# Performance work log

Hardware: AMD Instinct MI355X
Metric: run time of the kernel (lower is better)

The kernel has to match this reference:

```python
import jax, jax.numpy as jnp
import numpy as np

E, C, H, I = 8, 4096, 1024, 4096

def setup_inputs() -> dict:
    key = jax.random.key(0)
    k_x, k_g, k_u, k_d = jax.random.split(key, 4)
    scale_h = 1.0 / np.sqrt(H)
    scale_i = 1.0 / np.sqrt(I)
    return {
        "x_routed": jax.random.normal(k_x, (E, C, H), dtype=jnp.float32),
        "W_gate": jax.random.normal(k_g, (E, H, I), dtype=jnp.float32) * scale_h,
        "W_up": jax.random.normal(k_u, (E, H, I), dtype=jnp.float32) * scale_h,
        "W_down": jax.random.normal(k_d, (E, I, H), dtype=jnp.float32) * scale_i,
    }

def reference(x_routed, W_gate, W_up, W_down):
    # Per-expert SwiGLU MLP, batched over the expert axis as a grouped GEMM.
    # gate = silu(x @ Wg); up = x @ Wu; out = (gate * up) @ Wd
    gate = jax.nn.silu(jnp.einsum("ech,ehi->eci", x_routed, W_gate))
    up = jnp.einsum("ech,ehi->eci", x_routed, W_up)
    out = jnp.einsum("eci,eih->ech", gate * up, W_down)
    return out
```

## Files before the change

kernel.cpp:

```cpp
#include <hip/hip_runtime.h>
#include <hip/hip_bf16.h>
#include <stdint.h>
#include <stddef.h>

#define E_ 8
#define C_ 4096
#define H_ 1024
#define I_ 4096

typedef short s16;
typedef __attribute__((ext_vector_type(8))) short short8;
typedef __attribute__((ext_vector_type(4))) float f32x4;
typedef __attribute__((ext_vector_type(4))) float float4v;

__device__ __forceinline__ s16 f2bf(float f) {
  union { __hip_bfloat16 h; s16 s; } u;
  u.h = __float2bfloat16(f);
  return u.s;
}

__device__ __forceinline__ void gload16(const void* gsrc, void* ldst) {
  __builtin_amdgcn_global_load_lds(
      (const __attribute__((address_space(1))) void*)gsrc,
      (__attribute__((address_space(3))) void*)ldst, 16, 0, 0);
}

__global__ __launch_bounds__(256) void prep_kernel(
    const float* __restrict__ x, const float* __restrict__ Wg,
    const float* __restrict__ Wu, const float* __restrict__ Wd,
    s16* __restrict__ xb, s16* __restrict__ Wgu, s16* __restrict__ WdT)
{
  __shared__ float tile[64][65];
  const int t = threadIdx.x;
  const int z = blockIdx.z;
  const size_t e = blockIdx.y;

  if (z == 0) {
    size_t base = e * (size_t)C_ * H_ + ((size_t)blockIdx.x * 256 + t) * 16;
    for (int j = 0; j < 16; j += 8) {
      float4v v0 = *(const float4v*)(x + base + j);
      float4v v1 = *(const float4v*)(x + base + j + 4);
      s16 o[8];
      o[0] = f2bf(v0[0]); o[1] = f2bf(v0[1]); o[2] = f2bf(v0[2]); o[3] = f2bf(v0[3]);
      o[4] = f2bf(v1[0]); o[5] = f2bf(v1[1]); o[6] = f2bf(v1[2]); o[7] = f2bf(v1[3]);
      *(short8*)(xb + base + j) = *(short8*)o;
    }
    return;
  }

  const float* src; int Cc;
  if (z == 1)      { src = Wg + e * (size_t)H_ * I_; Cc = I_; }
  else if (z == 2) { src = Wu + e * (size_t)H_ * I_; Cc = I_; }
  else             { src = Wd + e * (size_t)H_ * I_; Cc = H_; }

  const int tpr  = Cc >> 6;
  const int trow = blockIdx.x / tpr;
  const int tcol = blockIdx.x % tpr;

  const int c = t & 63, rq = t >> 6;
  for (int i = 0; i < 16; ++i) {
    int r = rq * 16 + i;
    tile[r][c] = src[(size_t)(trow * 64 + r) * Cc + tcol * 64 + c];
  }
  __syncthreads();

  const int ro = t >> 2, cb = (t & 3) * 16;
  s16 o[16];
  for (int j = 0; j < 16; ++j) o[j] = f2bf(tile[cb + j][ro]);

  const int i0 = tcol * 64 + ro;
  s16* op;
  if (z == 3) {
    op = WdT + e * (size_t)H_ * I_ + (size_t)i0 * I_ + trow * 64 + cb;
  } else {
    int grow = ((i0 & ~15) << 1) + (i0 & 15) + ((z == 2) ? 16 : 0);
    op = Wgu + e * (size_t)2 * I_ * H_ + (size_t)grow * H_ + trow * 64 + cb;
  }
  *(short8*)op       = *(short8*)&o[0];
  *(short8*)(op + 8) = *(short8*)&o[8];
}

#define LDAF(B, MH, M, CX) \
  (*(const short8*)(shm + (B)*16384 + ((wm + (MH)*64 + (M)*16 + lr) << 6) + (CX)))
#define LDBF(B, N, CX) \
  (*(const short8*)(shm + 32768 + (B)*16384 + ((wn + (N)*16 + lr) << 6) + (CX)))

#define MFMA16(MH, A0, A1, A2, A3)                                                            \
  acc[(MH)*4+0][0] = __builtin_amdgcn_mfma_f32_16x16x32_bf16(A0, bf[0], acc[(MH)*4+0][0],0,0,0); \
  acc[(MH)*4+0][1] = __builtin_amdgcn_mfma_f32_16x16x32_bf16(A0, bf[1], acc[(MH)*4+0][1],0,0,0); \
  acc[(MH)*4+0][2] = __builtin_amdgcn_mfma_f32_16x16x32_bf16(A0, bf[2], acc[(MH)*4+0][2],0,0,0); \
  acc[(MH)*4+0][3] = __builtin_amdgcn_mfma_f32_16x16x32_bf16(A0, bf[3], acc[(MH)*4+0][3],0,0,0); \
  acc[(MH)*4+1][0] = __builtin_amdgcn_mfma_f32_16x16x32_bf16(A1, bf[0], acc[(MH)*4+1][0],0,0,0); \
  acc[(MH)*4+1][1] = __builtin_amdgcn_mfma_f32_16x16x32_bf16(A1, bf[1], acc[(MH)*4+1][1],0,0,0); \
  acc[(MH)*4+1][2] = __builtin_amdgcn_mfma_f32_16x16x32_bf16(A1, bf[2], acc[(MH)*4+1][2],0,0,0); \
  acc[(MH)*4+1][3] = __builtin_amdgcn_mfma_f32_16x16x32_bf16(A1, bf[3], acc[(MH)*4+1][3],0,0,0); \
  acc[(MH)*4+2][0] = __builtin_amdgcn_mfma_f32_16x16x32_bf16(A2, bf[0], acc[(MH)*4+2][0],0,0,0); \
  acc[(MH)*4+2][1] = __builtin_amdgcn_mfma_f32_16x16x32_bf16(A2, bf[1], acc[(MH)*4+2][1],0,0,0); \
  acc[(MH)*4+2][2] = __builtin_amdgcn_mfma_f32_16x16x32_bf16(A2, bf[2], acc[(MH)*4+2][2],0,0,0); \
  acc[(MH)*4+2][3] = __builtin_amdgcn_mfma_f32_16x16x32_bf16(A2, bf[3], acc[(MH)*4+2][3],0,0,0); \
  acc[(MH)*4+3][0] = __builtin_amdgcn_mfma_f32_16x16x32_bf16(A3, bf[0], acc[(MH)*4+3][0],0,0,0); \
  acc[(MH)*4+3][1] = __builtin_amdgcn_mfma_f32_16x16x32_bf16(A3, bf[1], acc[(MH)*4+3][1],0,0,0); \
  acc[(MH)*4+3][2] = __builtin_amdgcn_mfma_f32_16x16x32_bf16(A3, bf[2], acc[(MH)*4+3][2],0,0,0); \
  acc[(MH)*4+3][3] = __builtin_amdgcn_mfma_f32_16x16x32_bf16(A3, bf[3], acc[(MH)*4+3][3],0,0,0);

#define VMW4 asm volatile("s_waitcnt vmcnt(4)" ::: "memory");

#define PHASE(B, MH, CX, RDB, STMT, WV)                                      \
  {                                                                          \
    short8 af0 = LDAF(B, MH, 0, CX);                                         \
    short8 af1 = LDAF(B, MH, 1, CX);                                         \
    short8 af2 = LDAF(B, MH, 2, CX);                                         \
    short8 af3 = LDAF(B, MH, 3, CX);                                         \
    if (RDB) {                                                               \
      bf[0] = LDBF(B, 0, CX); bf[1] = LDBF(B, 1, CX);                        \
      bf[2] = LDBF(B, 2, CX); bf[3] = LDBF(B, 3, CX);                        \
    }                                                                        \
    STMT                                                                     \
    __builtin_amdgcn_sched_barrier(0);                                       \
    __builtin_amdgcn_s_barrier();                                            \
    asm volatile("s_waitcnt lgkmcnt(0)" ::: "memory");                       \
    __builtin_amdgcn_sched_barrier(0);                                       \
    __builtin_amdgcn_s_setprio(1);                                           \
    MFMA16(MH, af0, af1, af2, af3)                                           \
    __builtin_amdgcn_s_setprio(0);                                           \
    __builtin_amdgcn_sched_barrier(0);                                       \
    WV                                                                       \
    __builtin_amdgcn_s_barrier();                                            \
  }

template<bool GATEUP>
__global__ __launch_bounds__(512, 2) void gemm256(
    const s16* __restrict__ Abase, const s16* __restrict__ Bbase,
    s16* __restrict__ HOut, float* __restrict__ FOut)
{
  constexpr int K  = GATEUP ? H_ : I_;
  constexpr int NB = GATEUP ? 2 * I_ : H_;
  constexpr int NT = K / 64;
  constexpr int TN = NB / 256;
  constexpr int TM = C_ / 256;
  constexpr int NWG = TM * TN;

  __shared__ s16 shm[65536];

  const int tid  = threadIdx.x;
  const int wave = tid >> 6, lane = tid & 63;
  const int e    = blockIdx.z;

  const int bid = blockIdx.x;
  int bm, bn;
  if constexpr (GATEUP) {
    const int xcd = bid & 7;
    const int idx = bid >> 3;
    bn = (xcd & 3) * 8 + (idx & 7);
    bm = (xcd >> 2) * 8 + (idx >> 3);
  } else {
    const int swz = (bid & 7) * (NWG / 8) + (bid >> 3);
    bm = swz / TN; bn = swz % TN;
  }

  const s16* A = Abase + (size_t)e * C_ * K + (size_t)bm * 256 * K;
  const s16* B = Bbase + (size_t)e * NB * K + (size_t)bn * 256 * K;

  const int wm  = (wave >> 2) * 128;
  const int wn  = (wave & 3) * 64;
  const int lr  = lane & 15;
  const int lkb = (lane >> 4) * 8;
  const int xr  = (lr & 7) << 3;
  const int cx0 = lkb ^ xr;
  const int cx1 = (32 + lkb) ^ xr;

  const int srow = tid >> 3;
  const int scol = ((tid & 7) ^ (srow & 7)) * 8;
  const size_t stoff = (size_t)srow * K + scol;
  const int sdst = wave * 512;

  auto stageA = [&](int kt, int b) {
    #pragma unroll
    for (int h = 0; h < 2; ++h)
      #pragma unroll
      for (int l = 0; l < 2; ++l)
        gload16(A + (size_t)(h * 128 + l * 64) * K + (size_t)kt * 64 + stoff,
                shm + b * 16384 + h * 8192 + l * 4096 + sdst);
  };
  auto stageB = [&](int kt, int b) {
    #pragma unroll
    for (int h = 0; h < 2; ++h)
      #pragma unroll
      for (int l = 0; l < 2; ++l)
        gload16(B + (size_t)(h * 128 + l * 64) * K + (size_t)kt * 64 + stoff,
                shm + 32768 + b * 16384 + h * 8192 + l * 4096 + sdst);
  };

  f32x4 acc[8][4];
  #pragma unroll
  for (int m = 0; m < 8; ++m)
    #pragma unroll
    for (int n = 0; n < 4; ++n) acc[m][n] = (f32x4){0.f, 0.f, 0.f, 0.f};

  stageB(0, 0);
  stageA(0, 0);
  stageB(1, 1);
  asm volatile("s_waitcnt vmcnt(4)" ::: "memory");
  __builtin_amdgcn_sched_barrier(0);
  __builtin_amdgcn_s_barrier();

  short8 bf[4];
  for (int i = 0; i < NT / 2; ++i) {
    const int t1 = 2 * i + 1;
    const int t2 = (2 * i + 2 < NT) ? (2 * i + 2) : (NT - 1);
    const int t3 = (2 * i + 3 < NT) ? (2 * i + 3) : (NT - 1);
    PHASE(0, 0, cx0, 1, { stageA(t1, 1); }, )
    PHASE(0, 1, cx0, 0, {}, )
    PHASE(0, 0, cx1, 1, {}, )
    PHASE(0, 1, cx1, 0, { stageB(t2, 0); }, VMW4)
    PHASE(1, 0, cx0, 1, { stageA(t2, 0); }, )
    PHASE(1, 1, cx0, 0, {}, )
    PHASE(1, 0, cx1, 1, {}, )
    PHASE(1, 1, cx1, 0, { stageB(t3, 1); }, VMW4)
  }

  const int lq = (lane >> 4) * 4;
  if constexpr (GATEUP) {
    s16* Hp = HOut + (size_t)e * C_ * I_;
    const int ibase = bn * 128 + (wn >> 1);
    #pragma unroll
    for (int m = 0; m < 8; ++m) {
      const int row = bm * 256 + wm + m * 16 + lq;
      #pragma unroll
      for (int p = 0; p < 2; ++p) {
        const int col = ibase + p * 16 + lr;
        s16* hp = Hp + (size_t)row * I_ + col;
        #pragma unroll
        for (int j = 0; j < 4; ++j) {
          float g = acc[m][2 * p][j], u = acc[m][2 * p + 1][j];
          float sg = 1.0f / (1.0f + __expf(-g));
          hp[(size_t)j * I_] = f2bf(g * sg * u);
        }
      }
    }
  } else {
    float* Op = FOut + (size_t)e * C_ * H_;
    #pragma unroll
    for (int m = 0; m < 8; ++m) {
      const int row = bm * 256 + wm + m * 16 + lq;
      #pragma unroll
      for (int n = 0; n < 4; ++n) {
        const int col = bn * 256 + wn + n * 16 + lr;
        #pragma unroll
        for (int j = 0; j < 4; ++j)
          Op[(size_t)(row + j) * H_ + col] = acc[m][n][j];
      }
    }
  }
}

extern "C" void kernel_launch(void* const* d_in, const int* in_sizes, int n_in,
                              void* d_out, int out_size, void* d_ws, size_t ws_size,
                              hipStream_t stream) {
  const float* x  = (const float*)d_in[0];
  const float* Wg = (const float*)d_in[1];
  const float* Wu = (const float*)d_in[2];
  const float* Wd = (const float*)d_in[3];
  float* out = (float*)d_out;

  const size_t szX  = (size_t)C_ * H_;
  const size_t szGU = (size_t)2 * I_ * H_;
  const size_t szWd = (size_t)H_ * I_;
  const size_t szH  = (size_t)C_ * I_;

  const size_t needFull = 2 * E_ * (szX + szGU + szWd + szH);

  if (ws_size >= needFull) {
    s16* xb  = (s16*)d_ws;
    s16* Wgu = xb  + E_ * szX;
    s16* WdT = Wgu + E_ * szGU;
    s16* hbf = WdT + E_ * szWd;

    prep_kernel<<<dim3(1024, E_, 4), 256, 0, stream>>>(
        x, Wg, Wu, Wd, xb, Wgu, WdT);
    gemm256<true><<<dim3((C_/256)*(2*I_/256), 1, E_), 512, 0, stream>>>(
        xb, Wgu, hbf, nullptr);
    gemm256<false><<<dim3((C_/256)*(H_/256), 1, E_), 512, 0, stream>>>(
        hbf, WdT, nullptr, out);
  } else {
    s16* xb  = (s16*)d_ws;
    s16* Wgu = xb  + szX;
    s16* WdT = Wgu + szGU;
    s16* hbf = WdT + szWd;

    for (int e = 0; e < E_; ++e) {
      prep_kernel<<<dim3(1024, 1, 4), 256, 0, stream>>>(
          x + e * szX, Wg + e * szWd, Wu + e * szWd, Wd + e * szWd,
          xb, Wgu, WdT);
      gemm256<true><<<dim3((C_/256)*(2*I_/256), 1, 1), 512, 0, stream>>>(
          xb, Wgu, hbf, nullptr);
      gemm256<false><<<dim3((C_/256)*(H_/256), 1, 1), 512, 0, stream>>>(
          hbf, WdT, nullptr, out + e * szX);
    }
  }
}
```

Before: 965.4 us.

## Software-pipeline LDS fragment reads one phase ahead with partial lgkmcnt waits

After: 970.2 us. About the same (+0.5%).

```diff
diff --git a/kernel.cpp b/kernel.cpp
--- a/kernel.cpp
+++ b/kernel.cpp
@@ -85,43 +85,43 @@
 #define LDBF(B, N, CX) \
   (*(const short8*)(shm + 32768 + (B)*16384 + ((wn + (N)*16 + lr) << 6) + (CX)))
 
-#define MFMA16(MH, A0, A1, A2, A3)                                                            \
-  acc[(MH)*4+0][0] = __builtin_amdgcn_mfma_f32_16x16x32_bf16(A0, bf[0], acc[(MH)*4+0][0],0,0,0); \
-  acc[(MH)*4+0][1] = __builtin_amdgcn_mfma_f32_16x16x32_bf16(A0, bf[1], acc[(MH)*4+0][1],0,0,0); \
-  acc[(MH)*4+0][2] = __builtin_amdgcn_mfma_f32_16x16x32_bf16(A0, bf[2], acc[(MH)*4+0][2],0,0,0); \
-  acc[(MH)*4+0][3] = __builtin_amdgcn_mfma_f32_16x16x32_bf16(A0, bf[3], acc[(MH)*4+0][3],0,0,0); \
-  acc[(MH)*4+1][0] = __builtin_amdgcn_mfma_f32_16x16x32_bf16(A1, bf[0], acc[(MH)*4+1][0],0,0,0); \
-  acc[(MH)*4+1][1] = __builtin_amdgcn_mfma_f32_16x16x32_bf16(A1, bf[1], acc[(MH)*4+1][1],0,0,0); \
-  acc[(MH)*4+1][2] = __builtin_amdgcn_mfma_f32_16x16x32_bf16(A1, bf[2], acc[(MH)*4+1][2],0,0,0); \
-  acc[(MH)*4+1][3] = __builtin_amdgcn_mfma_f32_16x16x32_bf16(A1, bf[3], acc[(MH)*4+1][3],0,0,0); \
-  acc[(MH)*4+2][0] = __builtin_amdgcn_mfma_f32_16x16x32_bf16(A2, bf[0], acc[(MH)*4+2][0],0,0,0); \
-  acc[(MH)*4+2][1] = __builtin_amdgcn_mfma_f32_16x16x32_bf16(A2, bf[1], acc[(MH)*4+2][1],0,0,0); \
-  acc[(MH)*4+2][2] = __builtin_amdgcn_mfma_f32_16x16x32_bf16(A2, bf[2], acc[(MH)*4+2][2],0,0,0); \
-  acc[(MH)*4+2][3] = __builtin_amdgcn_mfma_f32_16x16x32_bf16(A2, bf[3], acc[(MH)*4+2][3],0,0,0); \
-  acc[(MH)*4+3][0] = __builtin_amdgcn_mfma_f32_16x16x32_bf16(A3, bf[0], acc[(MH)*4+3][0],0,0,0); \
-  acc[(MH)*4+3][1] = __builtin_amdgcn_mfma_f32_16x16x32_bf16(A3, bf[1], acc[(MH)*4+3][1],0,0,0); \
-  acc[(MH)*4+3][2] = __builtin_amdgcn_mfma_f32_16x16x32_bf16(A3, bf[2], acc[(MH)*4+3][2],0,0,0); \
-  acc[(MH)*4+3][3] = __builtin_amdgcn_mfma_f32_16x16x32_bf16(A3, bf[3], acc[(MH)*4+3][3],0,0,0);
+#define RD_A(DST, B, MH, CX)                                                 \
+  DST[0] = LDAF(B, MH, 0, CX); DST[1] = LDAF(B, MH, 1, CX);                  \
+  DST[2] = LDAF(B, MH, 2, CX); DST[3] = LDAF(B, MH, 3, CX);
+
+#define RD_B(DST, B, CX)                                                     \
+  DST[0] = LDBF(B, 0, CX); DST[1] = LDBF(B, 1, CX);                          \
+  DST[2] = LDBF(B, 2, CX); DST[3] = LDBF(B, 3, CX);
+
+#define MFMA16S(MH, AF, BF)                                                                     \
+  acc[(MH)*4+0][0] = __builtin_amdgcn_mfma_f32_16x16x32_bf16(AF[0], BF[0], acc[(MH)*4+0][0],0,0,0); \
+  acc[(MH)*4+0][1] = __builtin_amdgcn_mfma_f32_16x16x32_bf16(AF[0], BF[1], acc[(MH)*4+0][1],0,0,0); \
+  acc[(MH)*4+0][2] = __builtin_amdgcn_mfma_f32_16x16x32_bf16(AF[0], BF[2], acc[(MH)*4+0][2],0,0,0); \
+  acc[(MH)*4+0][3] = __builtin_amdgcn_mfma_f32_16x16x32_bf16(AF[0], BF[3], acc[(MH)*4+0][3],0,0,0); \
+  acc[(MH)*4+1][0] = __builtin_amdgcn_mfma_f32_16x16x32_bf16(AF[1], BF[0], acc[(MH)*4+1][0],0,0,0); \
+  acc[(MH)*4+1][1] = __builtin_amdgcn_mfma_f32_16x16x32_bf16(AF[1], BF[1], acc[(MH)*4+1][1],0,0,0); \
+  acc[(MH)*4+1][2] = __builtin_amdgcn_mfma_f32_16x16x32_bf16(AF[1], BF[2], acc[(MH)*4+1][2],0,0,0); \
+  acc[(MH)*4+1][3] = __builtin_amdgcn_mfma_f32_16x16x32_bf16(AF[1], BF[3], acc[(MH)*4+1][3],0,0,0); \
+  acc[(MH)*4+2][0] = __builtin_amdgcn_mfma_f32_16x16x32_bf16(AF[2], BF[0], acc[(MH)*4+2][0],0,0,0); \
+  acc[(MH)*4+2][1] = __builtin_amdgcn_mfma_f32_16x16x32_bf16(AF[2], BF[1], acc[(MH)*4+2][1],0,0,0); \
+  acc[(MH)*4+2][2] = __builtin_amdgcn_mfma_f32_16x16x32_bf16(AF[2], BF[2], acc[(MH)*4+2][2],0,0,0); \
+  acc[(MH)*4+2][3] = __builtin_amdgcn_mfma_f32_16x16x32_bf16(AF[2], BF[3], acc[(MH)*4+2][3],0,0,0); \
+  acc[(MH)*4+3][0] = __builtin_amdgcn_mfma_f32_16x16x32_bf16(AF[3], BF[0], acc[(MH)*4+3][0],0,0,0); \
+  acc[(MH)*4+3][1] = __builtin_amdgcn_mfma_f32_16x16x32_bf16(AF[3], BF[1], acc[(MH)*4+3][1],0,0,0); \
+  acc[(MH)*4+3][2] = __builtin_amdgcn_mfma_f32_16x16x32_bf16(AF[3], BF[2], acc[(MH)*4+3][2],0,0,0); \
+  acc[(MH)*4+3][3] = __builtin_amdgcn_mfma_f32_16x16x32_bf16(AF[3], BF[3], acc[(MH)*4+3][3],0,0,0);
 
 #define VMW4 asm volatile("s_waitcnt vmcnt(4)" ::: "memory");
 
-#define PHASE(B, MH, CX, RDB, STMT, WV)                                      \
+#define PH(TOP, LGKM, MH, AF, BF, WV)                                        \
   {                                                                          \
-    short8 af0 = LDAF(B, MH, 0, CX);                                         \
-    short8 af1 = LDAF(B, MH, 1, CX);                                         \
-    short8 af2 = LDAF(B, MH, 2, CX);                                         \
-    short8 af3 = LDAF(B, MH, 3, CX);                                         \
-    if (RDB) {                                                               \
-      bf[0] = LDBF(B, 0, CX); bf[1] = LDBF(B, 1, CX);                        \
-      bf[2] = LDBF(B, 2, CX); bf[3] = LDBF(B, 3, CX);                        \
-    }                                                                        \
-    STMT                                                                     \
+    TOP                                                                      \
     __builtin_amdgcn_sched_barrier(0);                                       \
     __builtin_amdgcn_s_barrier();                                            \
-    asm volatile("s_waitcnt lgkmcnt(0)" ::: "memory");                       \
+    asm volatile("s_waitcnt lgkmcnt(" #LGKM ")" ::: "memory");               \
     __builtin_amdgcn_sched_barrier(0);                                       \
     __builtin_amdgcn_s_setprio(1);                                           \
-    MFMA16(MH, af0, af1, af2, af3)                                           \
+    MFMA16S(MH, AF, BF)                                                      \
     __builtin_amdgcn_s_setprio(0);                                           \
     __builtin_amdgcn_sched_barrier(0);                                       \
     WV                                                                       \
@@ -204,19 +204,27 @@
   __builtin_amdgcn_sched_barrier(0);
   __builtin_amdgcn_s_barrier();
 
-  short8 bf[4];
+  short8 afA[4], afB[4], bfA[4], bfB[4];
   for (int i = 0; i < NT / 2; ++i) {
     const int t1 = 2 * i + 1;
     const int t2 = (2 * i + 2 < NT) ? (2 * i + 2) : (NT - 1);
     const int t3 = (2 * i + 3 < NT) ? (2 * i + 3) : (NT - 1);
-    PHASE(0, 0, cx0, 1, { stageA(t1, 1); }, )
-    PHASE(0, 1, cx0, 0, {}, )
-    PHASE(0, 0, cx1, 1, {}, )
-    PHASE(0, 1, cx1, 0, { stageB(t2, 0); }, VMW4)
-    PHASE(1, 0, cx0, 1, { stageA(t2, 0); }, )
-    PHASE(1, 1, cx0, 0, {}, )
-    PHASE(1, 0, cx1, 1, {}, )
-    PHASE(1, 1, cx1, 0, { stageB(t3, 1); }, VMW4)
+    PH({ RD_A(afA,0,0,cx0) RD_B(bfA,0,cx0) RD_A(afB,0,1,cx0) stageA(t1,1); },
+       4, 0, afA, bfA, )
+    PH({ RD_A(afA,0,0,cx1) RD_B(bfB,0,cx1) },
+       8, 1, afB, bfA, )
+    PH({ RD_A(afB,0,1,cx1) },
+       4, 0, afA, bfB, )
+    PH({ stageB(t2,0); },
+       0, 1, afB, bfB, VMW4)
+    PH({ RD_A(afA,1,0,cx0) RD_B(bfA,1,cx0) RD_A(afB,1,1,cx0) stageA(t2,0); },
+       4, 0, afA, bfA, )
+    PH({ RD_A(afA,1,0,cx1) RD_B(bfB,1,cx1) },
+       8, 1, afB, bfA, )
+    PH({ RD_A(afB,1,1,cx1) },
+       4, 0, afA, bfB, )
+    PH({ stageB(t3,1); },
+       0, 1, afB, bfB, VMW4)
   }
 
   const int lq = (lane >> 4) * 4;
```

## Process several N tiles per workgroup with continuous K-pipeline across tiles

Applied to the files above, without the earlier changes.

Measured after the change: 981.0 us. About the same (+1.6%).

```diff
diff --git a/kernel.cpp b/kernel.cpp
--- a/kernel.cpp
+++ b/kernel.cpp
@@ -128,17 +128,19 @@
     __builtin_amdgcn_s_barrier();                                            \
   }
 
-template<bool GATEUP>
+template<bool GATEUP, int NTILES>
 __global__ __launch_bounds__(512, 2) void gemm256(
     const s16* __restrict__ Abase, const s16* __restrict__ Bbase,
     s16* __restrict__ HOut, float* __restrict__ FOut)
 {
-  constexpr int K  = GATEUP ? H_ : I_;
-  constexpr int NB = GATEUP ? 2 * I_ : H_;
-  constexpr int NT = K / 64;
-  constexpr int TN = NB / 256;
-  constexpr int TM = C_ / 256;
-  constexpr int NWG = TM * TN;
+  constexpr int K     = GATEUP ? H_ : I_;
+  constexpr int NB    = GATEUP ? 2 * I_ : H_;
+  constexpr int NT    = K / 64;
+  constexpr int LOGNT = GATEUP ? 4 : 6;
+  constexpr int TN    = NB / 256;
+  constexpr int TNC   = TN / NTILES;
+  constexpr int TM    = C_ / 256;
+  constexpr int VMAX  = NTILES * NT - 1;
 
   __shared__ s16 shm[65536];
 
@@ -147,19 +149,19 @@
   const int e    = blockIdx.z;
 
   const int bid = blockIdx.x;
-  int bm, bn;
+  int bm, bnc;
   if constexpr (GATEUP) {
     const int xcd = bid & 7;
     const int idx = bid >> 3;
-    bn = (xcd & 3) * 8 + (idx & 7);
-    bm = (xcd >> 2) * 8 + (idx >> 3);
+    bnc = (xcd & 3) * 2 + (idx & 1);
+    bm  = (xcd >> 2) * 8 + (idx >> 1);
   } else {
-    const int swz = (bid & 7) * (NWG / 8) + (bid >> 3);
-    bm = swz / TN; bn = swz % TN;
-  }
-
-  const s16* A = Abase + (size_t)e * C_ * K + (size_t)bm * 256 * K;
-  const s16* B = Bbase + (size_t)e * NB * K + (size_t)bn * 256 * K;
+    const int swz = (bid & 7) * ((TM * TNC) / 8) + (bid >> 3);
+    bm = swz / TNC; bnc = swz % TNC;
+  }
+
+  const s16* A  = Abase + (size_t)e * C_ * K + (size_t)bm * 256 * K;
+  const s16* B0 = Bbase + (size_t)e * NB * K + (size_t)bnc * NTILES * 256 * K;
 
   const int wm  = (wave >> 2) * 128;
   const int wn  = (wave & 3) * 64;
@@ -174,7 +176,8 @@
   const size_t stoff = (size_t)srow * K + scol;
   const int sdst = wave * 512;
 
-  auto stageA = [&](int kt, int b) {
+  auto stageA = [&](int v, int b) {
+    const int kt = v & (NT - 1);
     #pragma unroll
     for (int h = 0; h < 2; ++h)
       #pragma unroll
@@ -182,12 +185,15 @@
         gload16(A + (size_t)(h * 128 + l * 64) * K + (size_t)kt * 64 + stoff,
                 shm + b * 16384 + h * 8192 + l * 4096 + sdst);
   };
-  auto stageB = [&](int kt, int b) {
+  auto stageB = [&](int v, int b) {
+    const int jb = v >> LOGNT;
+    const int kt = v & (NT - 1);
+    const s16* Bp = B0 + (size_t)jb * (256 * K);
     #pragma unroll
     for (int h = 0; h < 2; ++h)
       #pragma unroll
       for (int l = 0; l < 2; ++l)
-        gload16(B + (size_t)(h * 128 + l * 64) * K + (size_t)kt * 64 + stoff,
+        gload16(Bp + (size_t)(h * 128 + l * 64) * K + (size_t)kt * 64 + stoff,
                 shm + 32768 + b * 16384 + h * 8192 + l * 4096 + sdst);
   };
 
@@ -205,51 +211,62 @@
   __builtin_amdgcn_s_barrier();
 
   short8 bf[4];
-  for (int i = 0; i < NT / 2; ++i) {
-    const int t1 = 2 * i + 1;
-    const int t2 = (2 * i + 2 < NT) ? (2 * i + 2) : (NT - 1);
-    const int t3 = (2 * i + 3 < NT) ? (2 * i + 3) : (NT - 1);
-    PHASE(0, 0, cx0, 1, { stageA(t1, 1); }, )
-    PHASE(0, 1, cx0, 0, {}, )
-    PHASE(0, 0, cx1, 1, {}, )
-    PHASE(0, 1, cx1, 0, { stageB(t2, 0); }, VMW4)
-    PHASE(1, 0, cx0, 1, { stageA(t2, 0); }, )
-    PHASE(1, 1, cx0, 0, {}, )
-    PHASE(1, 0, cx1, 1, {}, )
-    PHASE(1, 1, cx1, 0, { stageB(t3, 1); }, VMW4)
-  }
-
   const int lq = (lane >> 4) * 4;
-  if constexpr (GATEUP) {
-    s16* Hp = HOut + (size_t)e * C_ * I_;
-    const int ibase = bn * 128 + (wn >> 1);
-    #pragma unroll
-    for (int m = 0; m < 8; ++m) {
-      const int row = bm * 256 + wm + m * 16 + lq;
-      #pragma unroll
-      for (int p = 0; p < 2; ++p) {
-        const int col = ibase + p * 16 + lr;
-        s16* hp = Hp + (size_t)row * I_ + col;
+
+  for (int j = 0; j < NTILES; ++j) {
+    for (int ii = 0; ii < NT / 2; ++ii) {
+      const int v  = j * NT + 2 * ii;
+      const int t1 = v + 1;
+      const int t2 = (v + 2 <= VMAX) ? v + 2 : VMAX;
+      const int t3 = (v + 3 <= VMAX) ? v + 3 : VMAX;
+      PHASE(0, 0, cx0, 1, { stageA(t1, 1); }, )
+      PHASE(0, 1, cx0, 0, {}, )
+      PHASE(0, 0, cx1, 1, {}, )
+      PHASE(0, 1, cx1, 0, { stageB(t2, 0); }, VMW4)
+      PHASE(1, 0, cx0, 1, { stageA(t2, 0); }, )
+      PHASE(1, 1, cx0, 0, {}, )
+      PHASE(1, 0, cx1, 1, {}, )
+      PHASE(1, 1, cx1, 0, { stageB(t3, 1); }, VMW4)
+    }
+
+    const int bn = bnc * NTILES + j;
+    if constexpr (GATEUP) {
+      s16* Hp = HOut + (size_t)e * C_ * I_;
+      const int ibase = bn * 128 + (wn >> 1);
+      #pragma unroll
+      for (int m = 0; m < 8; ++m) {
+        const int row = bm * 256 + wm + m * 16 + lq;
         #pragma unroll
-        for (int j = 0; j < 4; ++j) {
-          float g = acc[m][2 * p][j], u = acc[m][2 * p + 1][j];
-          float sg = 1.0f / (1.0f + __expf(-g));
-          hp[(size_t)j * I_] = f2bf(g * sg * u);
+        for (int p = 0; p < 2; ++p) {
+          const int col = ibase + p * 16 + lr;
+          s16* hp = Hp + (size_t)row * I_ + col;
+          #pragma unroll
+          for (int q = 0; q < 4; ++q) {
+            float g = acc[m][2 * p][q], u = acc[m][2 * p + 1][q];
+            float sg = 1.0f / (1.0f + __expf(-g));
+            hp[(size_t)q * I_] = f2bf(g * sg * u);
+          }
         }
       }
-    }
-  } else {
-    float* Op = FOut + (size_t)e * C_ * H_;
-    #pragma unroll
-    for (int m = 0; m < 8; ++m) {
-      const int row = bm * 256 + wm + m * 16 + lq;
-      #pragma unroll
-      for (int n = 0; n < 4; ++n) {
-        const int col = bn * 256 + wn + n * 16 + lr;
+    } else {
+      float* Op = FOut + (size_t)e * C_ * H_;
+      #pragma unroll
+      for (int m = 0; m < 8; ++m) {
+        const int row = bm * 256 + wm + m * 16 + lq;
         #pragma unroll
-        for (int j = 0; j < 4; ++j)
-          Op[(size_t)(row + j) * H_ + col] = acc[m][n][j];
+        for (int n = 0; n < 4; ++n) {
+          const int col = bn * 256 + wn + n * 16 + lr;
+          #pragma unroll
+          for (int q = 0; q < 4; ++q)
+            Op[(size_t)(row + q) * H_ + col] = acc[m][n][q];
+        }
       }
+    }
+    if (j + 1 < NTILES) {
+      #pragma unroll
+      for (int m = 0; m < 8; ++m)
+        #pragma unroll
+        for (int n = 0; n < 4; ++n) acc[m][n] = (f32x4){0.f, 0.f, 0.f, 0.f};
     }
   }
 }
@@ -270,6 +287,9 @@
 
   const size_t needFull = 2 * E_ * (szX + szGU + szWd + szH);
 
+  constexpr int GU_BLK = (C_ / 256) * ((2 * I_ / 256) / 4);
+  constexpr int DN_BLK = (C_ / 256) * ((H_ / 256) / 2);
+
   if (ws_size >= needFull) {
     s16* xb  = (s16*)d_ws;
     s16* Wgu = xb  + E_ * szX;
@@ -278,9 +298,9 @@
 
     prep_kernel<<<dim3(1024, E_, 4), 256, 0, stream>>>(
         x, Wg, Wu, Wd, xb, Wgu, WdT);
-    gemm256<true><<<dim3((C_/256)*(2*I_/256), 1, E_), 512, 0, stream>>>(
+    gemm256<true, 4><<<dim3(GU_BLK, 1, E_), 512, 0, stream>>>(
         xb, Wgu, hbf, nullptr);
-    gemm256<false><<<dim3((C_/256)*(H_/256), 1, E_), 512, 0, stream>>>(
+    gemm256<false, 2><<<dim3(DN_BLK, 1, E_), 512, 0, stream>>>(
         hbf, WdT, nullptr, out);
   } else {
     s16* xb  = (s16*)d_ws;
@@ -292,9 +312,9 @@
       prep_kernel<<<dim3(1024, 1, 4), 256, 0, stream>>>(
           x + e * szX, Wg + e * szWd, Wu + e * szWd, Wd + e * szWd,
           xb, Wgu, WdT);
-      gemm256<true><<<dim3((C_/256)*(2*I_/256), 1, 1), 512, 0, stream>>>(
+      gemm256<true, 4><<<dim3(GU_BLK, 1, 1), 512, 0, stream>>>(
           xb, Wgu, hbf, nullptr);
-      gemm256<false><<<dim3((C_/256)*(H_/256), 1, 1), 512, 0, stream>>>(
+      gemm256<false, 2><<<dim3(DN_BLK, 1, 1), 512, 0, stream>>>(
           hbf, WdT, nullptr, out + e * szX);
     }
   }
```
